# Performance work log

Hardware: AMD Instinct MI355X
Metric: run time of the kernel (lower is better)

## Reference

```python
import jax, jax.numpy as jnp
import numpy as np

B, T, N, D, K = 8, 64, 512, 64, 8
d = D // K  # per-head dim
NEG = -(2.0 ** 15) + 1.0  # -32767, as in source


def setup_inputs() -> dict:
    key = jax.random.key(0)
    ks = jax.random.split(key, 12)
    s = 0.05
    inp = {
        "x": jax.random.normal(ks[0], (B, T, N, D), dtype=jnp.float32),
        "ste": jax.random.normal(ks[1], (B, T, N, D), dtype=jnp.float32),
        "Wq": jax.random.normal(ks[2], (2 * D, D), dtype=jnp.float32) * s,
        "bq": jnp.zeros((D,), dtype=jnp.float32),
        "Wk": jax.random.normal(ks[3], (2 * D, D), dtype=jnp.float32) * s,
        "bk": jnp.zeros((D,), dtype=jnp.float32),
        "Wv": jax.random.normal(ks[4], (2 * D, D), dtype=jnp.float32) * s,
        "bv": jnp.zeros((D,), dtype=jnp.float32),
        "W1": jax.random.normal(ks[5], (D, D), dtype=jnp.float32) * s,
        "b1": jnp.zeros((D,), dtype=jnp.float32),
        "W2": jax.random.normal(ks[6], (D, D), dtype=jnp.float32) * s,
        "b2": jnp.zeros((D,), dtype=jnp.float32),
    }
    return inp


def reference(x, ste, Wq, bq, Wk, bk, Wv, bv, W1, b1, W2, b2):
    h = jnp.concatenate([x, ste], axis=-1)  # (B,T,N,2D)
    q = jax.nn.relu(jnp.einsum("btnf,fd->btnd", h, Wq) + bq)
    k = jax.nn.relu(jnp.einsum("btnf,fd->btnd", h, Wk) + bk)
    v = jax.nn.relu(jnp.einsum("btnf,fd->btnd", h, Wv) + bv)
    # split D into K heads of size d (torch split/cat over batch == head axis)
    q = q.reshape(B, T, N, K, d)
    k = k.reshape(B, T, N, K, d)
    v = v.reshape(B, T, N, K, d)
    scores = jnp.einsum("btnkd,bsnkd->bnkts", q, k) / jnp.sqrt(jnp.float32(d))
    causal = jnp.tril(jnp.ones((T, T), dtype=bool))  # (T,T)
    scores = jnp.where(causal, scores, jnp.float32(NEG))
    attn = jax.nn.softmax(scores, axis=-1)  # (B,N,K,T,T)
    out = jnp.einsum("bnkts,bsnkd->btnkd", attn, v).reshape(B, T, N, D)
    out = jax.nn.relu(jnp.einsum("btnd,de->btne", out, W1) + b1)
    out = jnp.einsum("btnd,de->btne", out, W2) + b2
    return out
```

## Files before the change

### kernel.cpp

```cpp
#include <hip/hip_runtime.h>


#define Bb 8
#define Tt 64
#define Nn 512
#define Dd 64

typedef unsigned short u16;
typedef unsigned int u32;
typedef __bf16 bf16x8 __attribute__((ext_vector_type(8)));
typedef float f32x4 __attribute__((ext_vector_type(4)));
typedef short s16x8 __attribute__((ext_vector_type(8)));

#define HS 136
#define WS 136
#define QS 72
#define PS 72

__device__ inline u16 f2bf(float f) {
    u32 x = __float_as_uint(f);
    x += 0x7fffu + ((x >> 16) & 1u);
    return (u16)(x >> 16);
}
__device__ inline bf16x8 ldf(const u16* p) { return *(const bf16x8*)p; }
__device__ inline bf16x8 zf8() {
    s16x8 z = {0, 0, 0, 0, 0, 0, 0, 0};
    return __builtin_bit_cast(bf16x8, z);
}

template<int KD, int MODE>
__device__ inline void mfma_gemm(const u16* __restrict__ A, int As,
                                 const u16* __restrict__ WT, int Ws,
                                 const float* __restrict__ bias,
                                 u16* __restrict__ O, int Os,
                                 float* __restrict__ G,
                                 int w, int lane, float scale) {
    const int l15 = lane & 15, qd = lane >> 4;
    f32x4 acc[4] = {{0,0,0,0},{0,0,0,0},{0,0,0,0},{0,0,0,0}};
    const u16* arow = &A[(16 * w + l15) * As];
#pragma unroll
    for (int k0 = 0; k0 < KD; k0 += 32) {
        bf16x8 af = ldf(arow + k0 + qd * 8);
#pragma unroll
        for (int ct = 0; ct < 4; ++ct) {
            bf16x8 bfr = ldf(&WT[(16 * ct + l15) * Ws + k0 + qd * 8]);
            acc[ct] = __builtin_amdgcn_mfma_f32_16x16x32_bf16(af, bfr, acc[ct], 0, 0, 0);
        }
    }
#pragma unroll
    for (int ct = 0; ct < 4; ++ct) {
        const int col = 16 * ct + l15;
        const float bv = bias[col];
#pragma unroll
        for (int r = 0; r < 4; ++r) {
            const int row = 16 * w + 4 * qd + r;
            float v = acc[ct][r] + bv;
            if (MODE != 2) v = fmaxf(v, 0.f);
            v *= scale;
            if (MODE == 0)      O[row * Os + col] = f2bf(v);
            else if (MODE == 1) O[col * Os + row] = f2bf(v);
            else                G[(size_t)row * (Nn * Dd) + col] = v;
        }
    }
}

template<int KD>
__device__ inline void stageW(const float* __restrict__ W, u16* __restrict__ wT,
                              int tid) {
    const int c = tid & 63;
    const int g = tid >> 6;
#pragma unroll
    for (int pass = 0; pass < KD / 16; ++pass) {
        const int f0 = (pass * 4 + g) * 4;
        ushort4 st;
        st.x = f2bf(W[(f0 + 0) * 64 + c]);
        st.y = f2bf(W[(f0 + 1) * 64 + c]);
        st.z = f2bf(W[(f0 + 2) * 64 + c]);
        st.w = f2bf(W[(f0 + 3) * 64 + c]);
        *(ushort4*)&wT[c * WS + f0] = st;
    }
}

__global__ __launch_bounds__(256)
void ta_fused_kernel(const float* __restrict__ x,  const float* __restrict__ ste,
                     const float* __restrict__ Wq, const float* __restrict__ bq,
                     const float* __restrict__ Wk, const float* __restrict__ bk,
                     const float* __restrict__ Wv, const float* __restrict__ bv,
                     const float* __restrict__ W1, const float* __restrict__ b1,
                     const float* __restrict__ W2, const float* __restrict__ b2,
                     float* __restrict__ out) {
    __shared__ __align__(16) u16 sm[31232];
    u16* h       = sm;
    u16* wT      = sm + 8704;
    u16* qb      = sm + 17408;
    u16* kb      = sm + 22016;
    u16* vT      = sm + 26624;
    u16* attnout = sm;
    u16* abuf    = qb;

    const int tid  = threadIdx.x;
    const int w    = tid >> 6;
    const int lane = tid & 63;
    const int l15  = lane & 15, qd = lane >> 4;
    const int bid  = blockIdx.x;
    const int b = bid >> 9, n = bid & 511;

    const float* xb = x   + (((size_t)b * Tt) * Nn + n) * Dd;
    const float* sb = ste + (((size_t)b * Tt) * Nn + n) * Dd;

#pragma unroll
    for (int l = 0; l < 8; ++l) {
        int idx = l * 256 + tid;
        int t = idx >> 5, p = idx & 31;
        const float* src = (p < 16) ? xb : sb;
        float4 vv = *(const float4*)(src + (size_t)t * (Nn * Dd) + (p & 15) * 4);
        ushort4 st;
        st.x = f2bf(vv.x); st.y = f2bf(vv.y); st.z = f2bf(vv.z); st.w = f2bf(vv.w);
        *(ushort4*)&h[t * HS + p * 4] = st;
    }
    __syncthreads();

    stageW<128>(Wq, wT, tid); __syncthreads();
    mfma_gemm<128, 0>(h, HS, wT, WS, bq, qb, QS, nullptr, w, lane, 0.35355339059327373f);
    __syncthreads();
    stageW<128>(Wk, wT, tid); __syncthreads();
    mfma_gemm<128, 0>(h, HS, wT, WS, bk, kb, QS, nullptr, w, lane, 1.f);
    __syncthreads();
    stageW<128>(Wv, wT, tid); __syncthreads();
    mfma_gemm<128, 1>(h, HS, wT, WS, bv, vT, QS, nullptr, w, lane, 1.f);
    __syncthreads();

    u16* pb = sm + 4608 + 1152 * w;
    const bf16x8 z8 = zf8();
#pragma unroll 1
    for (int h8 = 0; h8 < 64; h8 += 8) {
        bf16x8 af = (qd == 0) ? ldf(&qb[(16 * w + l15) * QS + h8]) : z8;
        f32x4 sv[4] = {{0,0,0,0},{0,0,0,0},{0,0,0,0},{0,0,0,0}};
#pragma unroll
        for (int ct = 0; ct < 4; ++ct) {
            bf16x8 bfr = (qd == 0) ? ldf(&kb[(16 * ct + l15) * QS + h8]) : z8;
            sv[ct] = __builtin_amdgcn_mfma_f32_16x16x32_bf16(af, bfr, sv[ct], 0, 0, 0);
        }
        const int tr = 16 * w + 4 * qd;
#pragma unroll
        for (int ct = 0; ct < 4; ++ct) {
            const int sc = 16 * ct + l15;
#pragma unroll
            for (int r = 0; r < 4; ++r)
                sv[ct][r] = (sc <= tr + r) ? __expf(sv[ct][r]) : 0.f;
        }
        f32x4 dsum = sv[0] + sv[1] + sv[2] + sv[3];
#pragma unroll
        for (int m = 1; m <= 8; m <<= 1) {
#pragma unroll
            for (int r = 0; r < 4; ++r)
                dsum[r] += __shfl_xor(dsum[r], m, 64);
        }
#pragma unroll
        for (int ct = 0; ct < 4; ++ct)
#pragma unroll
            for (int r = 0; r < 4; ++r)
                pb[(4 * qd + r) * PS + 16 * ct + l15] = f2bf(sv[ct][r]);
        f32x4 o = {0, 0, 0, 0};
#pragma unroll
        for (int k0 = 0; k0 < 64; k0 += 32) {
            bf16x8 pa = ldf(&pb[l15 * PS + k0 + qd * 8]);
            int vrow = h8 + (l15 & 7);
            bf16x8 vfr = (l15 < 8) ? ldf(&vT[vrow * QS + k0 + qd * 8]) : z8;
            o = __builtin_amdgcn_mfma_f32_16x16x32_bf16(pa, vfr, o, 0, 0, 0);
        }
        if (l15 < 8) {
#pragma unroll
            for (int r = 0; r < 4; ++r) {
                float inv = __builtin_amdgcn_rcpf(dsum[r]);
                attnout[(16 * w + 4 * qd + r) * QS + h8 + l15] = f2bf(o[r] * inv);
            }
        }
    }
    __syncthreads();

    stageW<64>(W1, wT, tid); __syncthreads();
    mfma_gemm<64, 0>(attnout, QS, wT, WS, b1, abuf, QS, nullptr, w, lane, 1.f);
    __syncthreads();
    stageW<64>(W2, wT, tid); __syncthreads();
    float* ob = out + (((size_t)b * Tt) * Nn + n) * Dd;
    mfma_gemm<64, 2>(abuf, QS, wT, WS, b2, nullptr, 0, ob, w, lane, 1.f);
}

extern "C" void kernel_launch(void* const* d_in, const int* in_sizes, int n_in,
                              void* d_out, int out_size, void* d_ws, size_t ws_size,
                              hipStream_t stream) {
    const float* x   = (const float*)d_in[0];
    const float* ste = (const float*)d_in[1];
    const float* Wq  = (const float*)d_in[2];
    const float* bq  = (const float*)d_in[3];
    const float* Wk  = (const float*)d_in[4];
    const float* bk  = (const float*)d_in[5];
    const float* Wv  = (const float*)d_in[6];
    const float* bv  = (const float*)d_in[7];
    const float* W1  = (const float*)d_in[8];
    const float* b1  = (const float*)d_in[9];
    const float* W2  = (const float*)d_in[10];
    const float* b2  = (const float*)d_in[11];
    float* out = (float*)d_out;

    hipLaunchKernelGGL(ta_fused_kernel, dim3(Bb * Nn), dim3(256), 0, stream,
                       x, ste, Wq, bq, Wk, bk, Wv, bv, W1, b1, W2, b2, out);
}
```

Baseline: 281.2 us.

## Pretranspose weights to bf16 workspace and read them from global memory

A small prep kernel converts and transposes all five weight matrices to bf16 in the workspace. The main kernel then reads weight fragments straight from global/L2 instead of staging them through shared memory, which drops the staging passes and several barriers. Q, K and V are computed in one fused loop. Bias is folded into the accumulator init, and exp2 is used with the log2e factor folded into the Q scale. The softmax denominator comes from an extra row of ones in V^T, which replaces the shuffle reduction. Shared memory shrinks, strides change, and launch bounds ask for 3 blocks per SM. The risk is more global-load latency inside the MFMA loops, in exchange for less LDS traffic and fewer synchronisations.

```diff
diff --git a/kernel.cpp b/kernel.cpp
--- a/kernel.cpp
+++ b/kernel.cpp
@@ -13,9 +13,15 @@
 typedef short s16x8 __attribute__((ext_vector_type(8)));
 
 #define HS 136
-#define WS 136
-#define QS 72
-#define PS 72
+#define QS 68
+
+#define QSCALE 0.51006977f
+
+#define WQ_OFF 0
+#define WK_OFF 8192
+#define WV_OFF 16384
+#define W1_OFF 24576
+#define W2_OFF 28672
 
 __device__ inline u16 f2bf(float f) {
     u32 x = __float_as_uint(f);
@@ -28,73 +34,73 @@
     return __builtin_bit_cast(bf16x8, z);
 }
 
-template<int KD, int MODE>
-__device__ inline void mfma_gemm(const u16* __restrict__ A, int As,
-                                 const u16* __restrict__ WT, int Ws,
-                                 const float* __restrict__ bias,
-                                 u16* __restrict__ O, int Os,
-                                 float* __restrict__ G,
-                                 int w, int lane, float scale) {
+__global__ __launch_bounds__(256)
+void prep_weights(const float* __restrict__ Wq, const float* __restrict__ Wk,
+                  const float* __restrict__ Wv, const float* __restrict__ W1,
+                  const float* __restrict__ W2, u16* __restrict__ ws) {
+    int t = blockIdx.x * 256 + threadIdx.x;
+    if (t < 24576) {
+        int m = t >> 13, r = t & 8191;
+        const float* W = (m == 0) ? Wq : (m == 1) ? Wk : Wv;
+        int f = r >> 6, c = r & 63;
+        ws[m * 8192 + c * 128 + f] = f2bf(W[r]);
+    } else {
+        int t2 = t - 24576;
+        int m = t2 >> 12, r = t2 & 4095;
+        const float* W = m ? W2 : W1;
+        int f = r >> 6, c = r & 63;
+        ws[24576 + m * 4096 + c * 64 + f] = f2bf(W[r]);
+    }
+}
+
+template<int MODE>
+__device__ inline void mfma_gemm64(const u16* __restrict__ A, int As,
+                                   const u16* __restrict__ Wg,
+                                   const float* __restrict__ bias,
+                                   u16* __restrict__ O, int Os,
+                                   float* __restrict__ G,
+                                   int w, int lane) {
     const int l15 = lane & 15, qd = lane >> 4;
-    f32x4 acc[4] = {{0,0,0,0},{0,0,0,0},{0,0,0,0},{0,0,0,0}};
+    f32x4 acc[4];
+#pragma unroll
+    for (int ct = 0; ct < 4; ++ct) {
+        float bv = bias[16 * ct + l15];
+        acc[ct] = (f32x4){bv, bv, bv, bv};
+    }
     const u16* arow = &A[(16 * w + l15) * As];
 #pragma unroll
-    for (int k0 = 0; k0 < KD; k0 += 32) {
+    for (int k0 = 0; k0 < 64; k0 += 32) {
         bf16x8 af = ldf(arow + k0 + qd * 8);
 #pragma unroll
         for (int ct = 0; ct < 4; ++ct) {
-            bf16x8 bfr = ldf(&WT[(16 * ct + l15) * Ws + k0 + qd * 8]);
+            bf16x8 bfr = ldf(&Wg[(16 * ct + l15) * 64 + k0 + qd * 8]);
             acc[ct] = __builtin_amdgcn_mfma_f32_16x16x32_bf16(af, bfr, acc[ct], 0, 0, 0);
         }
     }
 #pragma unroll
     for (int ct = 0; ct < 4; ++ct) {
         const int col = 16 * ct + l15;
-        const float bv = bias[col];
 #pragma unroll
         for (int r = 0; r < 4; ++r) {
             const int row = 16 * w + 4 * qd + r;
-            float v = acc[ct][r] + bv;
-            if (MODE != 2) v = fmaxf(v, 0.f);
-            v *= scale;
-            if (MODE == 0)      O[row * Os + col] = f2bf(v);
-            else if (MODE == 1) O[col * Os + row] = f2bf(v);
-            else                G[(size_t)row * (Nn * Dd) + col] = v;
-        }
-    }
-}
-
-template<int KD>
-__device__ inline void stageW(const float* __restrict__ W, u16* __restrict__ wT,
-                              int tid) {
-    const int c = tid & 63;
-    const int g = tid >> 6;
-#pragma unroll
-    for (int pass = 0; pass < KD / 16; ++pass) {
-        const int f0 = (pass * 4 + g) * 4;
-        ushort4 st;
-        st.x = f2bf(W[(f0 + 0) * 64 + c]);
-        st.y = f2bf(W[(f0 + 1) * 64 + c]);
-        st.z = f2bf(W[(f0 + 2) * 64 + c]);
-        st.w = f2bf(W[(f0 + 3) * 64 + c]);
-        *(ushort4*)&wT[c * WS + f0] = st;
-    }
-}
-
-__global__ __launch_bounds__(256)
+            float v = acc[ct][r];
+            if (MODE == 0) { v = fmaxf(v, 0.f); O[row * Os + col] = f2bf(v); }
+            else           { G[(size_t)row * (Nn * Dd) + col] = v; }
+        }
+    }
+}
+
+__global__ __launch_bounds__(256, 3)
 void ta_fused_kernel(const float* __restrict__ x,  const float* __restrict__ ste,
-                     const float* __restrict__ Wq, const float* __restrict__ bq,
-                     const float* __restrict__ Wk, const float* __restrict__ bk,
-                     const float* __restrict__ Wv, const float* __restrict__ bv,
-                     const float* __restrict__ W1, const float* __restrict__ b1,
-                     const float* __restrict__ W2, const float* __restrict__ b2,
+                     const float* __restrict__ bq, const float* __restrict__ bk,
+                     const float* __restrict__ bv_, const float* __restrict__ b1,
+                     const float* __restrict__ b2, const u16* __restrict__ wsr,
                      float* __restrict__ out) {
-    __shared__ __align__(16) u16 sm[31232];
+    __shared__ __align__(16) u16 sm[21828];
     u16* h       = sm;
-    u16* wT      = sm + 8704;
-    u16* qb      = sm + 17408;
-    u16* kb      = sm + 22016;
-    u16* vT      = sm + 26624;
+    u16* qb      = sm + 8704;
+    u16* kb      = sm + 13056;
+    u16* vT      = sm + 17408;
     u16* attnout = sm;
     u16* abuf    = qb;
 
@@ -107,6 +113,9 @@
 
     const float* xb = x   + (((size_t)b * Tt) * Nn + n) * Dd;
     const float* sb = ste + (((size_t)b * Tt) * Nn + n) * Dd;
+    const u16* wq = wsr + WQ_OFF;
+    const u16* wk = wsr + WK_OFF;
+    const u16* wv = wsr + WV_OFF;
 
 #pragma unroll
     for (int l = 0; l < 8; ++l) {
@@ -118,23 +127,54 @@
         st.x = f2bf(vv.x); st.y = f2bf(vv.y); st.z = f2bf(vv.z); st.w = f2bf(vv.w);
         *(ushort4*)&h[t * HS + p * 4] = st;
     }
+    if (tid < 64) vT[64 * QS + tid] = 0x3F80;
     __syncthreads();
 
-    stageW<128>(Wq, wT, tid); __syncthreads();
-    mfma_gemm<128, 0>(h, HS, wT, WS, bq, qb, QS, nullptr, w, lane, 0.35355339059327373f);
+    {
+        f32x4 qa[4], ka[4], va[4];
+#pragma unroll
+        for (int ct = 0; ct < 4; ++ct) {
+            int c = 16 * ct + l15;
+            float b0 = bq[c], b1v = bk[c], b2v = bv_[c];
+            qa[ct] = (f32x4){b0, b0, b0, b0};
+            ka[ct] = (f32x4){b1v, b1v, b1v, b1v};
+            va[ct] = (f32x4){b2v, b2v, b2v, b2v};
+        }
+        const u16* arow = &h[(16 * w + l15) * HS];
+#pragma unroll
+        for (int k0 = 0; k0 < 128; k0 += 32) {
+            bf16x8 af = ldf(arow + k0 + qd * 8);
+#pragma unroll
+            for (int ct = 0; ct < 4; ++ct) {
+                const int boff = (16 * ct + l15) * 128 + k0 + qd * 8;
+                bf16x8 bq8 = ldf(&wq[boff]);
+                qa[ct] = __builtin_amdgcn_mfma_f32_16x16x32_bf16(af, bq8, qa[ct], 0, 0, 0);
+                bf16x8 bk8 = ldf(&wk[boff]);
+                ka[ct] = __builtin_amdgcn_mfma_f32_16x16x32_bf16(af, bk8, ka[ct], 0, 0, 0);
+                bf16x8 bv8 = ldf(&wv[boff]);
+                va[ct] = __builtin_amdgcn_mfma_f32_16x16x32_bf16(af, bv8, va[ct], 0, 0, 0);
+            }
+        }
+#pragma unroll
+        for (int ct = 0; ct < 4; ++ct) {
+            const int col = 16 * ct + l15;
+#pragma unroll
+            for (int r = 0; r < 4; ++r) {
+                const int row = 16 * w + 4 * qd + r;
+                qb[row * QS + col] = f2bf(fmaxf(qa[ct][r], 0.f) * QSCALE);
+                kb[row * QS + col] = f2bf(fmaxf(ka[ct][r], 0.f));
+                vT[col * QS + row] = f2bf(fmaxf(va[ct][r], 0.f));
+            }
+        }
+    }
     __syncthreads();
-    stageW<128>(Wk, wT, tid); __syncthreads();
-    mfma_gemm<128, 0>(h, HS, wT, WS, bk, kb, QS, nullptr, w, lane, 1.f);
-    __syncthreads();
-    stageW<128>(Wv, wT, tid); __syncthreads();
-    mfma_gemm<128, 1>(h, HS, wT, WS, bv, vT, QS, nullptr, w, lane, 1.f);
-    __syncthreads();
-
-    u16* pb = sm + 4608 + 1152 * w;
+
+    u16* pb = sm + 4352 + 1088 * w;
     const bf16x8 z8 = zf8();
+    const u16* qrow = &qb[(16 * w + l15) * QS];
 #pragma unroll 1
     for (int h8 = 0; h8 < 64; h8 += 8) {
-        bf16x8 af = (qd == 0) ? ldf(&qb[(16 * w + l15) * QS + h8]) : z8;
+        bf16x8 af = (qd == 0) ? ldf(qrow + h8) : z8;
         f32x4 sv[4] = {{0,0,0,0},{0,0,0,0},{0,0,0,0},{0,0,0,0}};
 #pragma unroll
         for (int ct = 0; ct < 4; ++ct) {
@@ -147,44 +187,34 @@
             const int sc = 16 * ct + l15;
 #pragma unroll
             for (int r = 0; r < 4; ++r)
-                sv[ct][r] = (sc <= tr + r) ? __expf(sv[ct][r]) : 0.f;
-        }
-        f32x4 dsum = sv[0] + sv[1] + sv[2] + sv[3];
-#pragma unroll
-        for (int m = 1; m <= 8; m <<= 1) {
+                sv[ct][r] = (sc <= tr + r) ? exp2f(sv[ct][r]) : 0.f;
+        }
+#pragma unroll
+        for (int ct = 0; ct < 4; ++ct)
 #pragma unroll
             for (int r = 0; r < 4; ++r)
-                dsum[r] += __shfl_xor(dsum[r], m, 64);
-        }
-#pragma unroll
-        for (int ct = 0; ct < 4; ++ct)
-#pragma unroll
-            for (int r = 0; r < 4; ++r)
-                pb[(4 * qd + r) * PS + 16 * ct + l15] = f2bf(sv[ct][r]);
+                pb[(4 * qd + r) * QS + 16 * ct + l15] = f2bf(sv[ct][r]);
         f32x4 o = {0, 0, 0, 0};
 #pragma unroll
         for (int k0 = 0; k0 < 64; k0 += 32) {
-            bf16x8 pa = ldf(&pb[l15 * PS + k0 + qd * 8]);
-            int vrow = h8 + (l15 & 7);
-            bf16x8 vfr = (l15 < 8) ? ldf(&vT[vrow * QS + k0 + qd * 8]) : z8;
+            bf16x8 pa = ldf(&pb[l15 * QS + k0 + qd * 8]);
+            const int vrow = (l15 < 8) ? (h8 + l15) : 64;
+            bf16x8 vfr = (l15 <= 8) ? ldf(&vT[vrow * QS + k0 + qd * 8]) : z8;
             o = __builtin_amdgcn_mfma_f32_16x16x32_bf16(pa, vfr, o, 0, 0, 0);
         }
-        if (l15 < 8) {
-#pragma unroll
-            for (int r = 0; r < 4; ++r) {
-                float inv = __builtin_amdgcn_rcpf(dsum[r]);
-                attnout[(16 * w + 4 * qd + r) * QS + h8 + l15] = f2bf(o[r] * inv);
-            }
-        }
-    }
-    __syncthreads();
-
-    stageW<64>(W1, wT, tid); __syncthreads();
-    mfma_gemm<64, 0>(attnout, QS, wT, WS, b1, abuf, QS, nullptr, w, lane, 1.f);
-    __syncthreads();
-    stageW<64>(W2, wT, tid); __syncthreads();
+        const int dsrc = (lane & 48) | 8;
+#pragma unroll
+        for (int r = 0; r < 4; ++r) {
+            float den = __shfl(o[r], dsrc, 64);
+            if (l15 < 8)
+                attnout[(16 * w + 4 * qd + r) * QS + h8 + l15] =
+                    f2bf(o[r] * __builtin_amdgcn_rcpf(den));
+        }
+    }
+
+    mfma_gemm64<0>(attnout, QS, wsr + W1_OFF, b1, abuf, QS, nullptr, w, lane);
     float* ob = out + (((size_t)b * Tt) * Nn + n) * Dd;
-    mfma_gemm<64, 2>(abuf, QS, wT, WS, b2, nullptr, 0, ob, w, lane, 1.f);
+    mfma_gemm64<1>(abuf, QS, wsr + W2_OFF, b2, nullptr, 0, ob, w, lane);
 }
 
 extern "C" void kernel_launch(void* const* d_in, const int* in_sizes, int n_in,
@@ -203,7 +233,10 @@
     const float* W2  = (const float*)d_in[10];
     const float* b2  = (const float*)d_in[11];
     float* out = (float*)d_out;
-
+    u16* ws = (u16*)d_ws;
+
+    hipLaunchKernelGGL(prep_weights, dim3(128), dim3(256), 0, stream,
+                       Wq, Wk, Wv, W1, W2, ws);
     hipLaunchKernelGGL(ta_fused_kernel, dim3(Bb * Nn), dim3(256), 0, stream,
-                       x, ste, Wq, bq, Wk, bk, Wv, bv, W1, b1, W2, b2, out);
-}
+                       x, ste, bq, bk, bv, b1, b2, (const u16*)ws, out);
+}
```

Result: slower. 321.7 us (+14.4%).
